# Optimization experiments

Measured on AMD Instinct MI355X. Metric: run time of the kernel, lower is better.

Reference implementation:

```python
import jax, jax.numpy as jnp
import numpy as np

WINDOW = 129  # must be odd; matches init_kwargs


def setup_inputs() -> dict:
    key = jax.random.key(0)
    kq, kk, kv = jax.random.split(key, 3)
    shape = (1, 2048, 8, 64)  # (b, s, nh, h)
    return {
        "q": jax.random.normal(kq, shape, dtype=jnp.float32),
        "k": jax.random.normal(kk, shape, dtype=jnp.float32),
        "v": jax.random.normal(kv, shape, dtype=jnp.float32),
    }


def reference(q, k, v):
    # Sliding-window local attention, faithful to the pad+unfold torch module.
    b, s, nh, h = k.shape
    w = (WINDOW - 1) // 2
    W = 2 * w + 1
    scale = h ** (-0.5)
    qn = q * scale

    # zero-pad keys/values along the sequence dim by w on both sides
    kp = jnp.pad(k, ((0, 0), (w, w), (0, 0), (0, 0)))  # (b, s+2w, nh, h)
    vp = jnp.pad(v, ((0, 0), (w, w), (0, 0), (0, 0)))

    # idx[j, q] = j + q : padded key position for window offset j at query q
    idx = jnp.arange(W)[:, None] + jnp.arange(s)[None, :]  # (W, s)
    kw = kp[:, idx]  # (b, W, s, nh, h) -- unfolded key windows
    vw = vp[:, idx]  # (b, W, s, nh, h)

    # A[b, q, j, n] = <q[b,q,n,:], k_padded[b, j+q, n, :]>
    A = jnp.einsum('bqnh,bjqnh->bqjn', qn, kw)

    # mask out window slots pointing at padding (key pos j+q-w outside [0, s))
    valid = (idx >= w) & (idx < s + w)  # (W, s)
    mask_value = -jnp.finfo(A.dtype).max
    A = jnp.where(valid.T[None, :, :, None], A, mask_value)  # (1, s, W, 1) bcast

    # softmax over the window-offset axis (dim=-2 in the torch module)
    A = jax.nn.softmax(A, axis=2)

    # z[b, q, n, h] = sum_j A[b,q,j,n] * v_padded[b, j+q, n, h]
    z = jnp.einsum('bqjn,bjqnh->bqnh', A, vw)
    return z
```

## Files before the change

kernel.cpp:

```cpp
#include <hip/hip_runtime.h>
#include <math.h>


typedef __attribute__((ext_vector_type(8))) short short8;
typedef __attribute__((ext_vector_type(4))) float f32x4;

namespace {
constexpr int SEQ = 2048, NH = 8, HD = 64, WHALF = 64;
constexpr int TQ  = 64;
constexpr int ROWS = 192;
constexpr int KST  = 72;
constexpr int PST  = 200;
constexpr int VST  = 520;
constexpr int NHD  = NH * HD;
}

__device__ __forceinline__ ushort f2bf(float x) {
  return (ushort)((__float_as_uint(x) + 0x8000u) >> 16);
}
__device__ __forceinline__ float fexp2(float x) {
  float r;
  asm("v_exp_f32 %0, %1" : "=v"(r) : "v"(x));
  return r;
}
__device__ __forceinline__ float frcp(float x) {
  float r;
  asm("v_rcp_f32 %0, %1" : "=v"(r) : "v"(x));
  return r;
}

__global__ __launch_bounds__(1024, 4) void wattn_kernel(
    const float* __restrict__ q, const float* __restrict__ k,
    const float* __restrict__ v, float* __restrict__ out) {
  __shared__ __align__(16) short sK[ROWS * KST];
  __shared__ __align__(16) short sQ[TQ * KST];
  __shared__ __align__(16) short sP[TQ * PST];
  __shared__ __align__(16) short sV[24 * VST];
  __shared__ __align__(16) float sD[16 * 16];

  const int t = threadIdx.x;
  const int bid  = blockIdx.x;
  const int W    = (bid & 7) * 32 + (bid >> 3);
  const int tile = W & 31;
  const int n    = W >> 5;
  const int q0   = tile * TQ;
  const size_t hb = (size_t)n * HD;

  const int w = t >> 6, lane = t & 63, lq = lane & 15, lg = lane >> 4;
  const int qw = w & 3;
  const int ht = w >> 2;

  #pragma unroll
  for (int it = 0; it < 3; ++it) {
    int f = t + it * 1024;
    int row = f >> 4, c16 = f & 15;
    int grow = q0 - WHALF + row;
    int cg = min(max(grow, 0), SEQ - 1);
    float4 kv = *(const float4*)(k + (size_t)cg * NHD + hb + c16 * 4);
    uint lo = (uint)f2bf(kv.x) | ((uint)f2bf(kv.y) << 16);
    uint hi = (uint)f2bf(kv.z) | ((uint)f2bf(kv.w) << 16);
    *(uint2*)&sK[row * KST + c16 * 4] = make_uint2(lo, hi);
  }
  {
    int row = t >> 4, c16 = t & 15;
    float4 qv = *(const float4*)(q + (size_t)(q0 + row) * NHD + hb + c16 * 4);
    uint lo = (uint)f2bf(qv.x) | ((uint)f2bf(qv.y) << 16);
    uint hi = (uint)f2bf(qv.z) | ((uint)f2bf(qv.w) << 16);
    *(uint2*)&sQ[row * KST + c16 * 4] = make_uint2(lo, hi);
  }

  {
    const int hcol = t & 63;
    const int u = t >> 6;
    auto stage_vg = [&](int g) {
      short8 pk;
      #pragma unroll
      for (int j = 0; j < 8; ++j) {
        int grow = q0 - WHALF + g * 8 + j;
        int cg = min(max(grow, 0), SEQ - 1);
        pk[j] = (short)f2bf(v[(size_t)cg * NHD + hb + hcol]);
      }
      *(short8*)&sV[g * VST + hcol * 8] = pk;
    };
    stage_vg(u);
    if (u < 8) stage_vg(16 + u);
  }

  __syncthreads();

  const int qd = qw * 16 + lq;
  const short8 qf0 = *(const short8*)&sQ[qd * KST + 8 * lg];
  const short8 qf1 = *(const short8*)&sQ[qd * KST + 32 + 8 * lg];

  const float EXPC = 0.125f * 1.4426950408889634f;
  const int rlo = max(qd, WHALF - q0);
  const int rhi = min(qd + 2 * WHALF, SEQ - 1 + WHALF - q0);

  auto do_tile = [&](int rt, float& ws) {
    const int rb = rt * 16;
    short8 kf0 = *(const short8*)&sK[(rb + lq) * KST + 8 * lg];
    short8 kf1 = *(const short8*)&sK[(rb + lq) * KST + 32 + 8 * lg];
    f32x4 acc = {0.f, 0.f, 0.f, 0.f};
    acc = __builtin_amdgcn_mfma_f32_16x16x32_bf16(kf0, qf0, acc, 0, 0, 0);
    acc = __builtin_amdgcn_mfma_f32_16x16x32_bf16(kf1, qf1, acc, 0, 0, 0);
    ushort pb[4];
    #pragma unroll
    for (int r = 0; r < 4; ++r) {
      int row = rb + 4 * lg + r;
      bool valid = (row >= rlo) && (row <= rhi);
      float p = valid ? fexp2((float)acc[r] * EXPC) : 0.f;
      ws += p;
      pb[r] = f2bf(p);
    }
    uint lo = (uint)pb[0] | ((uint)pb[1] << 16);
    uint hi = (uint)pb[2] | ((uint)pb[3] << 16);
    *(uint2*)&sP[qd * PST + rb + 4 * lg] = make_uint2(lo, hi);
  };

  float ws = 0.f;
  do_tile(ht, ws);
  do_tile(ht + 4, ws);
  do_tile(ht + 8, ws);

  ws += __shfl_xor(ws, 16);
  ws += __shfl_xor(ws, 32);
  if (lane < 16) sD[w * 16 + lane] = ws;

  __syncthreads();

  float4 dsum = make_float4(0.f, 0.f, 0.f, 0.f);
  #pragma unroll
  for (int j = 0; j < 4; ++j) {
    float4 dp = *(const float4*)(sD + (qw + 4 * j) * 16 + 4 * lg);
    dsum.x += dp.x; dsum.y += dp.y; dsum.z += dp.z; dsum.w += dp.w;
  }

  f32x4 acc = {0.f, 0.f, 0.f, 0.f};
  #pragma unroll
  for (int kc = 0; kc < 6; ++kc) {
    short8 pa = *(const short8*)&sP[qd * PST + kc * 32 + 8 * lg];
    short8 vb = *(const short8*)&sV[(kc * 4 + lg) * VST + (ht * 16 + lq) * 8];
    acc = __builtin_amdgcn_mfma_f32_16x16x32_bf16(pa, vb, acc, 0, 0, 0);
  }

  float di[4] = {frcp(dsum.x), frcp(dsum.y), frcp(dsum.z), frcp(dsum.w)};
  float* op = out + (size_t)(q0 + qw * 16 + 4 * lg) * NHD + hb + ht * 16 + lq;
  #pragma unroll
  for (int r = 0; r < 4; ++r)
    op[(size_t)r * NHD] = (float)acc[r] * di[r];
}

extern "C" void kernel_launch(void* const* d_in, const int* in_sizes, int n_in,
                              void* d_out, int out_size, void* d_ws, size_t ws_size,
                              hipStream_t stream) {
  const float* q = (const float*)d_in[0];
  const float* k = (const float*)d_in[1];
  const float* v = (const float*)d_in[2];
  float* out = (float*)d_out;
  dim3 grid((SEQ / TQ) * NH);
  hipLaunchKernelGGL(wattn_kernel, grid, dim3(1024), 0, stream, q, k, v, out);
}
```

Baseline: 12.05 us.

## Defer V conversion and LDS store past QK softmax to overlap global loads

V values are now loaded into registers before the first barrier, but their bf16 conversion and LDS store are deferred until after the QK^T/exp stage. The global V load latency can then overlap the first MFMA phase instead of stalling the first barrier. The __syncthreads calls are replaced with a custom barrier that waits only on LDS counters (lgkmcnt), so outstanding global V loads do not block it. This costs 16 extra registers per thread and depends on the compiler inserting the correct vmcnt wait before the deferred stores.

```diff
diff --git a/kernel.cpp b/kernel.cpp
--- a/kernel.cpp
+++ b/kernel.cpp
@@ -27,6 +27,11 @@
   float r;
   asm("v_rcp_f32 %0, %1" : "=v"(r) : "v"(x));
   return r;
+}
+__device__ __forceinline__ void wg_barrier() {
+  asm volatile("s_waitcnt lgkmcnt(0)" ::: "memory");
+  __builtin_amdgcn_s_barrier();
+  __builtin_amdgcn_sched_barrier(0);
 }
 
 __global__ __launch_bounds__(1024, 4) void wattn_kernel(
@@ -69,24 +74,24 @@
     *(uint2*)&sQ[row * KST + c16 * 4] = make_uint2(lo, hi);
   }
 
-  {
-    const int hcol = t & 63;
-    const int u = t >> 6;
-    auto stage_vg = [&](int g) {
-      short8 pk;
-      #pragma unroll
-      for (int j = 0; j < 8; ++j) {
-        int grow = q0 - WHALF + g * 8 + j;
-        int cg = min(max(grow, 0), SEQ - 1);
-        pk[j] = (short)f2bf(v[(size_t)cg * NHD + hb + hcol]);
-      }
-      *(short8*)&sV[g * VST + hcol * 8] = pk;
-    };
-    stage_vg(u);
-    if (u < 8) stage_vg(16 + u);
+  const int hcol = t & 63;
+  const int u = t >> 6;
+  const float* vbase = v + hb + hcol;
+  float va[8], va2[8];
+  #pragma unroll
+  for (int j = 0; j < 8; ++j) {
+    int cg = min(max(q0 - WHALF + u * 8 + j, 0), SEQ - 1);
+    va[j] = vbase[(size_t)cg * NHD];
+  }
+  if (u < 8) {
+    #pragma unroll
+    for (int j = 0; j < 8; ++j) {
+      int cg = min(max(q0 - WHALF + (16 + u) * 8 + j, 0), SEQ - 1);
+      va2[j] = vbase[(size_t)cg * NHD];
+    }
   }
 
-  __syncthreads();
+  wg_barrier();
 
   const int qd = qw * 16 + lq;
   const short8 qf0 = *(const short8*)&sQ[qd * KST + 8 * lg];
@@ -122,11 +127,23 @@
   do_tile(ht + 4, ws);
   do_tile(ht + 8, ws);
 
+  {
+    short8 pk;
+    #pragma unroll
+    for (int j = 0; j < 8; ++j) pk[j] = (short)f2bf(va[j]);
+    *(short8*)&sV[u * VST + hcol * 8] = pk;
+    if (u < 8) {
+      #pragma unroll
+      for (int j = 0; j < 8; ++j) pk[j] = (short)f2bf(va2[j]);
+      *(short8*)&sV[(16 + u) * VST + hcol * 8] = pk;
+    }
+  }
+
   ws += __shfl_xor(ws, 16);
   ws += __shfl_xor(ws, 32);
   if (lane < 16) sD[w * 16 + lane] = ws;
 
-  __syncthreads();
+  wg_barrier();
 
   float4 dsum = make_float4(0.f, 0.f, 0.f, 0.f);
   #pragma unroll
```

Measured after the change: 10.82 us. 1.11x faster.

## Halve block to 512 threads, doubling per-wave work and loading Q directly

Applied to the files above, without the earlier changes.

Block size drops from 1024 to 512 threads. Each wave now computes six score tiles and two output column tiles, reusing its P fragment across both PV MFMAs. Q fragments are loaded straight from global memory into registers and converted there, which removes the sQ shared buffer and its staging. The aim is to cut block-level sync cost and LDS use and to reuse the P operand, at the price of more serial work per wave and less parallelism in flight.

```diff
diff --git a/kernel.cpp b/kernel.cpp
--- a/kernel.cpp
+++ b/kernel.cpp
@@ -18,6 +18,14 @@
 __device__ __forceinline__ ushort f2bf(float x) {
   return (ushort)((__float_as_uint(x) + 0x8000u) >> 16);
 }
+__device__ __forceinline__ short8 cvt8(float4 a, float4 b) {
+  short8 r;
+  r[0] = (short)f2bf(a.x); r[1] = (short)f2bf(a.y);
+  r[2] = (short)f2bf(a.z); r[3] = (short)f2bf(a.w);
+  r[4] = (short)f2bf(b.x); r[5] = (short)f2bf(b.y);
+  r[6] = (short)f2bf(b.z); r[7] = (short)f2bf(b.w);
+  return r;
+}
 __device__ __forceinline__ float fexp2(float x) {
   float r;
   asm("v_exp_f32 %0, %1" : "=v"(r) : "v"(x));
@@ -29,14 +37,13 @@
   return r;
 }
 
-__global__ __launch_bounds__(1024, 4) void wattn_kernel(
+__global__ __launch_bounds__(512, 4) void wattn_kernel(
     const float* __restrict__ q, const float* __restrict__ k,
     const float* __restrict__ v, float* __restrict__ out) {
   __shared__ __align__(16) short sK[ROWS * KST];
-  __shared__ __align__(16) short sQ[TQ * KST];
   __shared__ __align__(16) short sP[TQ * PST];
   __shared__ __align__(16) short sV[24 * VST];
-  __shared__ __align__(16) float sD[16 * 16];
+  __shared__ __align__(16) float sD[8 * 16];
 
   const int t = threadIdx.x;
   const int bid  = blockIdx.x;
@@ -48,11 +55,11 @@
 
   const int w = t >> 6, lane = t & 63, lq = lane & 15, lg = lane >> 4;
   const int qw = w & 3;
-  const int ht = w >> 2;
+  const int h2 = w >> 2;
 
   #pragma unroll
-  for (int it = 0; it < 3; ++it) {
-    int f = t + it * 1024;
+  for (int it = 0; it < 6; ++it) {
+    int f = t + it * 512;
     int row = f >> 4, c16 = f & 15;
     int grow = q0 - WHALF + row;
     int cg = min(max(grow, 0), SEQ - 1);
@@ -61,17 +68,9 @@
     uint hi = (uint)f2bf(kv.z) | ((uint)f2bf(kv.w) << 16);
     *(uint2*)&sK[row * KST + c16 * 4] = make_uint2(lo, hi);
   }
-  {
-    int row = t >> 4, c16 = t & 15;
-    float4 qv = *(const float4*)(q + (size_t)(q0 + row) * NHD + hb + c16 * 4);
-    uint lo = (uint)f2bf(qv.x) | ((uint)f2bf(qv.y) << 16);
-    uint hi = (uint)f2bf(qv.z) | ((uint)f2bf(qv.w) << 16);
-    *(uint2*)&sQ[row * KST + c16 * 4] = make_uint2(lo, hi);
-  }
 
   {
-    const int hcol = t & 63;
-    const int u = t >> 6;
+    const int hcol = lane;
     auto stage_vg = [&](int g) {
       short8 pk;
       #pragma unroll
@@ -82,15 +81,17 @@
       }
       *(short8*)&sV[g * VST + hcol * 8] = pk;
     };
-    stage_vg(u);
-    if (u < 8) stage_vg(16 + u);
+    stage_vg(w);
+    stage_vg(w + 8);
+    stage_vg(w + 16);
   }
 
   __syncthreads();
 
   const int qd = qw * 16 + lq;
-  const short8 qf0 = *(const short8*)&sQ[qd * KST + 8 * lg];
-  const short8 qf1 = *(const short8*)&sQ[qd * KST + 32 + 8 * lg];
+  const float* qp = q + (size_t)(q0 + qd) * NHD + hb + lg * 8;
+  const short8 qf0 = cvt8(*(const float4*)(qp + 0), *(const float4*)(qp + 4));
+  const short8 qf1 = cvt8(*(const float4*)(qp + 32), *(const float4*)(qp + 36));
 
   const float EXPC = 0.125f * 1.4426950408889634f;
   const int rlo = max(qd, WHALF - q0);
@@ -118,9 +119,12 @@
   };
 
   float ws = 0.f;
-  do_tile(ht, ws);
-  do_tile(ht + 4, ws);
-  do_tile(ht + 8, ws);
+  do_tile(h2,      ws);
+  do_tile(h2 + 2,  ws);
+  do_tile(h2 + 4,  ws);
+  do_tile(h2 + 6,  ws);
+  do_tile(h2 + 8,  ws);
+  do_tile(h2 + 10, ws);
 
   ws += __shfl_xor(ws, 16);
   ws += __shfl_xor(ws, 32);
@@ -130,24 +134,30 @@
 
   float4 dsum = make_float4(0.f, 0.f, 0.f, 0.f);
   #pragma unroll
-  for (int j = 0; j < 4; ++j) {
+  for (int j = 0; j < 2; ++j) {
     float4 dp = *(const float4*)(sD + (qw + 4 * j) * 16 + 4 * lg);
     dsum.x += dp.x; dsum.y += dp.y; dsum.z += dp.z; dsum.w += dp.w;
   }
 
-  f32x4 acc = {0.f, 0.f, 0.f, 0.f};
+  f32x4 acc0 = {0.f, 0.f, 0.f, 0.f};
+  f32x4 acc1 = {0.f, 0.f, 0.f, 0.f};
   #pragma unroll
   for (int kc = 0; kc < 6; ++kc) {
-    short8 pa = *(const short8*)&sP[qd * PST + kc * 32 + 8 * lg];
-    short8 vb = *(const short8*)&sV[(kc * 4 + lg) * VST + (ht * 16 + lq) * 8];
-    acc = __builtin_amdgcn_mfma_f32_16x16x32_bf16(pa, vb, acc, 0, 0, 0);
+    short8 pa  = *(const short8*)&sP[qd * PST + kc * 32 + 8 * lg];
+    short8 vb0 = *(const short8*)&sV[(kc * 4 + lg) * VST + ((h2)     * 16 + lq) * 8];
+    short8 vb1 = *(const short8*)&sV[(kc * 4 + lg) * VST + ((h2 + 2) * 16 + lq) * 8];
+    acc0 = __builtin_amdgcn_mfma_f32_16x16x32_bf16(pa, vb0, acc0, 0, 0, 0);
+    acc1 = __builtin_amdgcn_mfma_f32_16x16x32_bf16(pa, vb1, acc1, 0, 0, 0);
   }
 
   float di[4] = {frcp(dsum.x), frcp(dsum.y), frcp(dsum.z), frcp(dsum.w)};
-  float* op = out + (size_t)(q0 + qw * 16 + 4 * lg) * NHD + hb + ht * 16 + lq;
+  float* op0 = out + (size_t)(q0 + qw * 16 + 4 * lg) * NHD + hb + h2 * 16 + lq;
+  float* op1 = op0 + 32;
   #pragma unroll
-  for (int r = 0; r < 4; ++r)
-    op[(size_t)r * NHD] = (float)acc[r] * di[r];
+  for (int r = 0; r < 4; ++r) {
+    op0[(size_t)r * NHD] = (float)acc0[r] * di[r];
+    op1[(size_t)r * NHD] = (float)acc1[r] * di[r];
+  }
 }
 
 extern "C" void kernel_launch(void* const* d_in, const int* in_sizes, int n_in,
@@ -158,5 +168,5 @@
   const float* v = (const float*)d_in[2];
   float* out = (float*)d_out;
   dim3 grid((SEQ / TQ) * NH);
-  hipLaunchKernelGGL(wattn_kernel, grid, dim3(1024), 0, stream, q, k, v, out);
+  hipLaunchKernelGGL(wattn_kernel, grid, dim3(512), 0, stream, q, k, v, out);
 }
```

Measured after the change: 10.72 us. -11.1%, faster.
